# Optimization experiments

Hardware: AMD Instinct MI355X
Metric: run time of the kernel (lower is better)

The kernel has to match this reference:

```python
import jax, jax.numpy as jnp
import numpy as np

B, N, QD, OBJ_F, CONV_F = 16384, 6, 11, 10, 100
G_IN = 2 * CONV_F + QD  # 211


def _init_linear(key, fan_in, fan_out):
    kw, kb = jax.random.split(key)
    bound = 1.0 / np.sqrt(fan_in)
    W = jax.random.uniform(kw, (fan_in, fan_out), jnp.float32, -bound, bound)
    b = jax.random.uniform(kb, (fan_out,), jnp.float32, -bound, bound)
    return W, b


def setup_inputs() -> dict:
    key = jax.random.key(0)
    ks = jax.random.split(key, 13)
    tabs = jax.random.normal(ks[0], (B, N, OBJ_F), jnp.float32)
    qst = jax.random.normal(ks[1], (B, QD), jnp.float32)
    Wi1, bi1 = _init_linear(ks[2], 10, 256)
    Wi2, bi2 = _init_linear(ks[3], 256, 128)
    Wi3, bi3 = _init_linear(ks[4], 128, 100)
    Wg1, bg1 = _init_linear(ks[5], G_IN, 256)
    Wg2, bg2 = _init_linear(ks[6], 256, 256)
    Wg3, bg3 = _init_linear(ks[7], 256, 256)
    Wg4, bg4 = _init_linear(ks[8], 256, 256)
    Wf, bf = _init_linear(ks[9], 256, 256)
    Wo1, bo1 = _init_linear(ks[10], 256, 256)
    Wo2, bo2 = _init_linear(ks[11], 256, 10)
    return dict(tabs=tabs, qst=qst, Wi1=Wi1, bi1=bi1, Wi2=Wi2, bi2=bi2,
                Wi3=Wi3, bi3=bi3, Wg1=Wg1, bg1=bg1, Wg2=Wg2, bg2=bg2,
                Wg3=Wg3, bg3=bg3, Wg4=Wg4, bg4=bg4, Wf=Wf, bf=bf,
                Wo1=Wo1, bo1=bo1, Wo2=Wo2, bo2=bo2)


def reference(tabs, qst, Wi1, bi1, Wi2, bi2, Wi3, bi3,
              Wg1, bg1, Wg2, bg2, Wg3, bg3, Wg4, bg4,
              Wf, bf, Wo1, bo1, Wo2, bo2):
    relu = jax.nn.relu
    mb = tabs.shape[0]
    # object encoder: [B, N, 10] -> [B, N, 100]
    x = relu(tabs @ Wi1 + bi1)
    x = relu(x @ Wi2 + bi2)
    x = x @ Wi3 + bi3
    # x_j side carries the question: [B, N, 111]
    xq = jnp.concatenate([x, jnp.broadcast_to(qst[:, None, :], (mb, N, QD))], axis=-1)
    # pairwise features: pair (i, j) = [x[j], x[i], qst]  (matches torch repeat/cat)
    x_i = jnp.broadcast_to(x[:, None, :, :], (mb, N, N, CONV_F))
    x_j = jnp.broadcast_to(xq[:, :, None, :], (mb, N, N, CONV_F + QD))
    pair = jnp.concatenate([x_i, x_j], axis=-1).reshape(mb * N * N, G_IN)
    # g MLP over all pairs
    h = relu(pair @ Wg1 + bg1)
    h = relu(h @ Wg2 + bg2)
    h = relu(h @ Wg3 + bg3)
    h = relu(h @ Wg4 + bg4)
    # sum-pool over the 36 pairs
    g = h.reshape(mb, N * N, 256).sum(axis=1)
    # f MLP + output head (dropout treated as identity / eval mode)
    f = relu(g @ Wf + bf)
    o = relu(f @ Wo1 + bo1)
    logits = o @ Wo2 + bo2
    return jax.nn.log_softmax(logits, axis=1)
```

## Files before the change

### kernel.cpp

```cpp
#include <hip/hip_runtime.h>
#include <hip/hip_bf16.h>
#include <stdint.h>

typedef __attribute__((ext_vector_type(8))) __bf16 bf16x8;
typedef __attribute__((ext_vector_type(8))) short short8v;
typedef __attribute__((ext_vector_type(4))) short short4v;
typedef __attribute__((ext_vector_type(4))) float f32x4;
typedef __attribute__((ext_vector_type(2))) uint32_t u32x2;
typedef __attribute__((ext_vector_type(4))) uint32_t u32x4;

__device__ __forceinline__ float bf2f(short u) {
  return __builtin_bit_cast(float, (uint32_t)((uint32_t)(uint16_t)u << 16));
}
__device__ __forceinline__ short f2bf(float f) {
  uint32_t x = __builtin_bit_cast(uint32_t, f);
  x += 0x7FFFu + ((x >> 16) & 1u);
  return (short)(x >> 16);
}
__device__ __forceinline__ uint32_t cvtpk(float lo, float hi) {
  uint32_t r;
  asm("v_cvt_pk_bf16_f32 %0, %1, %2" : "=v"(r) : "v"(lo), "v"(hi));
  return r;
}
__device__ __forceinline__ f32x4 mfma16(short8v a, short8v b, f32x4 c) {
  return __builtin_amdgcn_mfma_f32_16x16x32_bf16(
      __builtin_bit_cast(bf16x8, a), __builtin_bit_cast(bf16x8, b), c, 0, 0, 0);
}
__device__ __forceinline__ int swz256(int row, int col) {
  return row * 256 + (col ^ ((row & 15) << 3));
}
__device__ __forceinline__ int swz128(int row, int col) {
  return row * 128 + (col ^ ((row & 15) << 3));
}

struct PPDesc { const float* src; short* dst; int Ks, Ns, KT, NT, tile_base; };
struct PPArgs { PPDesc d[11]; int n_desc; int total_tiles; };

__global__ void prepack_all(PPArgs args) {
  int idx = blockIdx.x * 256 + threadIdx.x;
  int tile = idx >> 6;
  if (tile >= args.total_tiles) return;
  int lane = idx & 63;
  int e = 0;
  while (e + 1 < args.n_desc && args.d[e + 1].tile_base <= tile) ++e;
  const PPDesc D = args.d[e];
  int t = tile - D.tile_base;
  int kt = t % D.KT, nt = t / D.KT;
  int n = nt * 16 + (lane & 15);
  int kbase = kt * 32 + ((lane >> 4) * 8);
  short8v o;
#pragma unroll
  for (int j = 0; j < 8; ++j) {
    int k = kbase + j;
    o[j] = f2bf((k < D.Ks && n < D.Ns) ? D.src[k * D.Ns + n] : 0.f);
  }
  *(short8v*)&D.dst[((size_t)t * 64 + lane) * 8] = o;
}

__global__ void qb_kernel(const float* __restrict__ qst, const float* __restrict__ Wg1,
                          const float* __restrict__ bg1, float* __restrict__ qb) {
  int c = threadIdx.x;
  int b0 = blockIdx.x * 32;
  float wcol[11];
#pragma unroll
  for (int k = 0; k < 11; ++k) wcol[k] = Wg1[(200 + k) * 256 + c];
  float bias = bg1[c];
#pragma unroll 1
  for (int bb = 0; bb < 32; ++bb) {
    int b = b0 + bb;
    float acc = bias;
#pragma unroll
    for (int k = 0; k < 11; ++k) acc += qst[b * 11 + k] * wcol[k];
    qb[b * 256 + c] = acc;
  }
}

__launch_bounds__(256, 3)
__global__ void enc_kernel(const float* __restrict__ tabs,
    const float* __restrict__ bi1, const float* __restrict__ bi2, const float* __restrict__ bi3,
    const short* __restrict__ Wi1p, const short* __restrict__ Wi2p, const short* __restrict__ Wi3p,
    const short* __restrict__ Wap, const short* __restrict__ Wbp,
    short* __restrict__ u_g, short* __restrict__ v_g) {
  __shared__ __align__(16) short sIn[64 * 32];
  __shared__ __align__(16) short sH1[64 * 256];
  __shared__ __align__(16) short sH2[64 * 128];
  short* sX = sH1;
  const int tid = threadIdx.x;
  const int lane = tid & 63, w = tid >> 6, quad = lane >> 4, ll = lane & 15;
  const int xl = ll << 3;
  const int obj0 = blockIdx.x * 64;

  for (int idx = tid; idx < 64 * 32; idx += 256) {
    int r = idx >> 5, k = idx & 31;
    float v = (k < 10) ? tabs[(obj0 + r) * 10 + k] : 0.f;
    sIn[idx] = f2bf(v);
  }
  __syncthreads();

  {
    f32x4 acc[4][4];
#pragma unroll
    for (int mi = 0; mi < 4; ++mi) {
      f32x4 b4 = *(const f32x4*)&bi1[(w * 4 + mi) * 16 + quad * 4];
#pragma unroll
      for (int nt = 0; nt < 4; ++nt) acc[mi][nt] = b4;
    }
    short8v wv[4];
#pragma unroll
    for (int mi = 0; mi < 4; ++mi)
      wv[mi] = *(const short8v*)&Wi1p[((w * 4 + mi) * 64 + lane) * 8];
#pragma unroll
    for (int nt = 0; nt < 4; ++nt) {
      short8v a = *(const short8v*)&sIn[(nt * 16 + ll) * 32 + quad * 8];
#pragma unroll
      for (int mi = 0; mi < 4; ++mi) acc[mi][nt] = mfma16(wv[mi], a, acc[mi][nt]);
    }
#pragma unroll
    for (int mi = 0; mi < 4; ++mi) {
      int c0 = (w * 4 + mi) * 16 + quad * 4;
#pragma unroll
      for (int nt = 0; nt < 4; ++nt) {
        int row = nt * 16 + ll;
        f32x4 a = acc[mi][nt];
        u32x2 o = {cvtpk(fmaxf(a[0], 0.f), fmaxf(a[1], 0.f)),
                   cvtpk(fmaxf(a[2], 0.f), fmaxf(a[3], 0.f))};
        *(u32x2*)&sH1[row * 256 + (c0 ^ ((row & 15) << 3))] = o;
      }
    }
  }
  __syncthreads();

  {
    f32x4 acc[2][4];
#pragma unroll
    for (int mi = 0; mi < 2; ++mi) {
      f32x4 b4 = *(const f32x4*)&bi2[(w * 2 + mi) * 16 + quad * 4];
#pragma unroll
      for (int nt = 0; nt < 4; ++nt) acc[mi][nt] = b4;
    }
#pragma unroll 1
    for (int kt = 0; kt < 8; ++kt) {
      short8v wv[2];
#pragma unroll
      for (int mi = 0; mi < 2; ++mi)
        wv[mi] = *(const short8v*)&Wi2p[(((w * 2 + mi) * 8 + kt) * 64 + lane) * 8];
#pragma unroll
      for (int nt = 0; nt < 4; ++nt) {
        short8v a = *(const short8v*)&sH1[(nt * 16 + ll) * 256 + ((kt * 32 + quad * 8) ^ xl)];
#pragma unroll
        for (int mi = 0; mi < 2; ++mi) acc[mi][nt] = mfma16(wv[mi], a, acc[mi][nt]);
      }
    }
    __syncthreads();
#pragma unroll
    for (int mi = 0; mi < 2; ++mi) {
      int c0 = (w * 2 + mi) * 16 + quad * 4;
#pragma unroll
      for (int nt = 0; nt < 4; ++nt) {
        int row = nt * 16 + ll;
        f32x4 a = acc[mi][nt];
        u32x2 o = {cvtpk(fmaxf(a[0], 0.f), fmaxf(a[1], 0.f)),
                   cvtpk(fmaxf(a[2], 0.f), fmaxf(a[3], 0.f))};
        *(u32x2*)&sH2[row * 128 + (c0 ^ ((row & 15) << 3))] = o;
      }
    }
  }
  __syncthreads();

  {
    f32x4 acc[4][2] = {};
#pragma unroll 1
    for (int kt = 0; kt < 4; ++kt) {
      short8v b[2];
#pragma unroll
      for (int ni = 0; ni < 2; ++ni)
        b[ni] = *(const short8v*)&Wi3p[(((w * 2 + ni) * 4 + kt) * 64 + lane) * 8];
#pragma unroll
      for (int mt = 0; mt < 4; ++mt) {
        short8v a = *(const short8v*)&sH2[(mt * 16 + ll) * 128 + ((kt * 32 + quad * 8) ^ xl)];
#pragma unroll
        for (int ni = 0; ni < 2; ++ni) acc[mt][ni] = mfma16(a, b[ni], acc[mt][ni]);
      }
    }
#pragma unroll
    for (int ni = 0; ni < 2; ++ni) {
      int col = (w * 2 + ni) * 16 + ll;
      float bias = (col < 100) ? bi3[col] : 0.f;
#pragma unroll
      for (int mt = 0; mt < 4; ++mt)
#pragma unroll
        for (int r = 0; r < 4; ++r) {
          int row = mt * 16 + quad * 4 + r;
          float vv = (col < 100) ? (acc[mt][ni][r] + bias) : 0.f;
          sX[swz128(row, col)] = f2bf(vv);
        }
    }
  }
  __syncthreads();

#pragma unroll 1
  for (int pass = 0; pass < 2; ++pass) {
    const short* Wp = pass ? Wbp : Wap;
    short* outg = pass ? v_g : u_g;
    f32x4 acc[4][4] = {};
#pragma unroll 1
    for (int kt = 0; kt < 4; ++kt) {
      short8v wv[4];
#pragma unroll
      for (int mi = 0; mi < 4; ++mi)
        wv[mi] = *(const short8v*)&Wp[(((w * 4 + mi) * 4 + kt) * 64 + lane) * 8];
#pragma unroll
      for (int nt = 0; nt < 4; ++nt) {
        short8v xb = *(const short8v*)&sX[(nt * 16 + ll) * 128 + ((kt * 32 + quad * 8) ^ xl)];
#pragma unroll
        for (int mi = 0; mi < 4; ++mi) acc[mi][nt] = mfma16(wv[mi], xb, acc[mi][nt]);
      }
    }
#pragma unroll
    for (int mi = 0; mi < 4; ++mi) {
      int c0 = (w * 4 + mi) * 16 + quad * 4;
#pragma unroll
      for (int nt = 0; nt < 4; ++nt) {
        int obj = obj0 + nt * 16 + ll;
        f32x4 a = acc[mi][nt];
        u32x2 o = {cvtpk(a[0], a[1]), cvtpk(a[2], a[3])};
        *(u32x2*)&outg[(size_t)obj * 256 + c0] = o;
      }
    }
  }
}

__launch_bounds__(512, 4)
__global__ void pair_kernel(const short* __restrict__ u_g, const short* __restrict__ v_g,
    const float* __restrict__ qbp,
    const short* __restrict__ Wg2p, const short* __restrict__ Wg3p, const short* __restrict__ Wg4p,
    const float* __restrict__ bg2, const float* __restrict__ bg3, const float* __restrict__ bg4,
    float* __restrict__ g_g) {
  __shared__ __align__(16) short sH[80 * 256];
  const int tid = threadIdx.x;
  const int lane = tid & 63, w = tid >> 6, quad = lane >> 4, ll = lane & 15;
  const int xl = ll << 3;
  const int b0 = blockIdx.x * 2;

  if (tid < 256) *(short8v*)&sH[72 * 256 + tid * 8] = short8v{};

#pragma unroll 1
  for (int it = 0; it < 5; ++it) {
    int vi = it * 512 + tid;
    if (vi < 2304) {
      int row = vi >> 5, c8 = (vi & 31) * 8;
      int bb = row / 36, p = row - bb * 36;
      int i2 = p / 6, j2 = p - i2 * 6;
      short8v u8 = *(const short8v*)&u_g[(size_t)((b0 + bb) * 6 + j2) * 256 + c8];
      short8v v8 = *(const short8v*)&v_g[(size_t)((b0 + bb) * 6 + i2) * 256 + c8];
      f32x4 qa = *(const f32x4*)&qbp[(size_t)(b0 + bb) * 256 + c8];
      f32x4 qc = *(const f32x4*)&qbp[(size_t)(b0 + bb) * 256 + c8 + 4];
      float m[8];
#pragma unroll
      for (int e = 0; e < 4; ++e) m[e] = fmaxf(bf2f(u8[e]) + bf2f(v8[e]) + qa[e], 0.f);
#pragma unroll
      for (int e = 0; e < 4; ++e) m[4 + e] = fmaxf(bf2f(u8[4 + e]) + bf2f(v8[4 + e]) + qc[e], 0.f);
      u32x4 o = {cvtpk(m[0], m[1]), cvtpk(m[2], m[3]), cvtpk(m[4], m[5]), cvtpk(m[6], m[7])};
      *(u32x4*)&sH[row * 256 + (c8 ^ ((row & 15) << 3))] = o;
    }
  }
  __syncthreads();

  f32x4 acc[5][2];

#pragma unroll 1
  for (int L = 0; L < 2; ++L) {
    const short* __restrict__ Wp = L ? Wg3p : Wg2p;
    const float* __restrict__ bp = L ? bg3 : bg2;
#pragma unroll
    for (int ni = 0; ni < 2; ++ni) {
      f32x4 b4 = *(const f32x4*)&bp[(w * 2 + ni) * 16 + quad * 4];
#pragma unroll
      for (int mt = 0; mt < 5; ++mt) acc[mt][ni] = b4;
    }
#pragma unroll 1
    for (int kt = 0; kt < 8; ++kt) {
      short8v wv[2];
#pragma unroll
      for (int ni = 0; ni < 2; ++ni)
        wv[ni] = *(const short8v*)&Wp[(((w * 2 + ni) * 8 + kt) * 64 + lane) * 8];
#pragma unroll
      for (int mt = 0; mt < 5; ++mt) {
        short8v h = *(const short8v*)&sH[(mt * 16 + ll) * 256 + ((kt * 32 + quad * 8) ^ xl)];
#pragma unroll
        for (int ni = 0; ni < 2; ++ni) acc[mt][ni] = mfma16(wv[ni], h, acc[mt][ni]);
      }
    }
    __syncthreads();
#pragma unroll
    for (int ni = 0; ni < 2; ++ni) {
      int c0 = (w * 2 + ni) * 16 + quad * 4;
#pragma unroll
      for (int mt = 0; mt < 5; ++mt) {
        int row = mt * 16 + ll;
        f32x4 a = acc[mt][ni];
        u32x2 o = {cvtpk(fmaxf(a[0], 0.f), fmaxf(a[1], 0.f)),
                   cvtpk(fmaxf(a[2], 0.f), fmaxf(a[3], 0.f))};
        *(u32x2*)&sH[row * 256 + (c0 ^ ((row & 15) << 3))] = o;
      }
    }
    __syncthreads();
  }

  {
#pragma unroll
    for (int ni = 0; ni < 2; ++ni) {
      float b = bg4[(w * 2 + ni) * 16 + ll];
#pragma unroll
      for (int mt = 0; mt < 5; ++mt) acc[mt][ni] = f32x4{b, b, b, b};
    }
#pragma unroll 1
    for (int kt = 0; kt < 8; ++kt) {
      short8v bv[2];
#pragma unroll
      for (int ni = 0; ni < 2; ++ni)
        bv[ni] = *(const short8v*)&Wg4p[(((w * 2 + ni) * 8 + kt) * 64 + lane) * 8];
#pragma unroll
      for (int mt = 0; mt < 5; ++mt) {
        short8v a = *(const short8v*)&sH[(mt * 16 + ll) * 256 + ((kt * 32 + quad * 8) ^ xl)];
#pragma unroll
        for (int ni = 0; ni < 2; ++ni) acc[mt][ni] = mfma16(a, bv[ni], acc[mt][ni]);
      }
    }
#pragma unroll
    for (int ni = 0; ni < 2; ++ni) {
      int col = (w * 2 + ni) * 16 + ll;
      float s0 = 0.f, s1 = 0.f;
#pragma unroll
      for (int mt = 0; mt < 5; ++mt) {
        int rbase = mt * 16 + quad * 4;
        float t = 0.f;
#pragma unroll
        for (int r = 0; r < 4; ++r) t += fmaxf(acc[mt][ni][r], 0.f);
        if (rbase < 36) s0 += t;
        else if (rbase < 72) s1 += t;
      }
      s0 += __shfl_xor(s0, 16, 64); s0 += __shfl_xor(s0, 32, 64);
      s1 += __shfl_xor(s1, 16, 64); s1 += __shfl_xor(s1, 32, 64);
      if (quad == 0) {
        g_g[(size_t)(b0 + 0) * 256 + col] = s0;
        g_g[(size_t)(b0 + 1) * 256 + col] = s1;
      }
    }
  }
}

template<int MT>
__device__ __forceinline__ void gemmMx256(const short* sInp, short* sOut,
    const short* __restrict__ Wp, const float* __restrict__ bias,
    int w, int lane, int quad, int ll, int xl) {
  f32x4 acc[MT][4] = {};
#pragma unroll 1
  for (int kt = 0; kt < 8; ++kt) {
    short8v b[4];
#pragma unroll
    for (int ni = 0; ni < 4; ++ni)
      b[ni] = *(const short8v*)&Wp[(((w * 4 + ni) * 8 + kt) * 64 + lane) * 8];
#pragma unroll
    for (int mt = 0; mt < MT; ++mt) {
      short8v a = *(const short8v*)&sInp[(mt * 16 + ll) * 256 + ((kt * 32 + quad * 8) ^ xl)];
#pragma unroll
      for (int ni = 0; ni < 4; ++ni) acc[mt][ni] = mfma16(a, b[ni], acc[mt][ni]);
    }
  }
#pragma unroll
  for (int ni = 0; ni < 4; ++ni) {
    int col = (w * 4 + ni) * 16 + ll;
    float bv = bias[col];
#pragma unroll
    for (int mt = 0; mt < MT; ++mt)
#pragma unroll
      for (int r = 0; r < 4; ++r) {
        int row = mt * 16 + quad * 4 + r;
        sOut[swz256(row, col)] = f2bf(fmaxf(acc[mt][ni][r] + bv, 0.f));
      }
  }
}

__launch_bounds__(256, 4)
__global__ void head_kernel(const float* __restrict__ g_g,
    const short* __restrict__ Wfp, const float* __restrict__ bf_,
    const short* __restrict__ Wo1p, const float* __restrict__ bo1,
    const short* __restrict__ Wo2p, const float* __restrict__ bo2,
    float* __restrict__ outp) {
  __shared__ __align__(16) short sA[32 * 256];
  __shared__ __align__(16) short sB[32 * 256];
  __shared__ float sL[32 * 16];
  const int tid = threadIdx.x;
  const int lane = tid & 63, w = tid >> 6, quad = lane >> 4, ll = lane & 15;
  const int xl = ll << 3;
  const int b0 = blockIdx.x * 32;

#pragma unroll 1
  for (int it = 0; it < 8; ++it) {
    int vi = it * 256 + tid;
    int row = vi >> 6, c4 = (vi & 63) * 4;
    f32x4 gv = *(const f32x4*)&g_g[(size_t)(b0 + row) * 256 + c4];
    short4v o;
#pragma unroll
    for (int e = 0; e < 4; ++e) o[e] = f2bf(gv[e]);
    *(short4v*)&sA[row * 256 + (c4 ^ ((row & 15) << 3))] = o;
  }
  __syncthreads();
  gemmMx256<2>(sA, sB, Wfp, bf_, w, lane, quad, ll, xl);
  __syncthreads();
  gemmMx256<2>(sB, sA, Wo1p, bo1, w, lane, quad, ll, xl);
  __syncthreads();
  if (w < 2) {
    f32x4 acc = {};
#pragma unroll 1
    for (int kt = 0; kt < 8; ++kt) {
      short8v b = *(const short8v*)&Wo2p[(kt * 64 + lane) * 8];
      short8v a = *(const short8v*)&sA[(w * 16 + ll) * 256 + ((kt * 32 + quad * 8) ^ xl)];
      acc = mfma16(a, b, acc);
    }
#pragma unroll
    for (int r = 0; r < 4; ++r) {
      int row = w * 16 + quad * 4 + r;
      sL[row * 16 + ll] = acc[r] + ((ll < 10) ? bo2[ll] : 0.f);
    }
  }
  __syncthreads();
  if (tid < 32) {
    float m = -1e30f;
#pragma unroll
    for (int c = 0; c < 10; ++c) m = fmaxf(m, sL[tid * 16 + c]);
    float s = 0.f;
#pragma unroll
    for (int c = 0; c < 10; ++c) s += expf(sL[tid * 16 + c] - m);
    float ls = logf(s) + m;
#pragma unroll
    for (int c = 0; c < 10; ++c) outp[(size_t)(b0 + tid) * 10 + c] = sL[tid * 16 + c] - ls;
  }
}

extern "C" void kernel_launch(void* const* d_in, const int* in_sizes, int n_in,
                              void* d_out, int out_size, void* d_ws, size_t ws_size,
                              hipStream_t stream) {
  const float* tabs = (const float*)d_in[0];
  const float* qst  = (const float*)d_in[1];
  const float* Wi1 = (const float*)d_in[2];  const float* bi1 = (const float*)d_in[3];
  const float* Wi2 = (const float*)d_in[4];  const float* bi2 = (const float*)d_in[5];
  const float* Wi3 = (const float*)d_in[6];  const float* bi3 = (const float*)d_in[7];
  const float* Wg1 = (const float*)d_in[8];  const float* bg1 = (const float*)d_in[9];
  const float* Wg2 = (const float*)d_in[10]; const float* bg2 = (const float*)d_in[11];
  const float* Wg3 = (const float*)d_in[12]; const float* bg3 = (const float*)d_in[13];
  const float* Wg4 = (const float*)d_in[14]; const float* bg4 = (const float*)d_in[15];
  const float* Wf  = (const float*)d_in[16]; const float* bf_ = (const float*)d_in[17];
  const float* Wo1 = (const float*)d_in[18]; const float* bo1 = (const float*)d_in[19];
  const float* Wo2 = (const float*)d_in[20]; const float* bo2 = (const float*)d_in[21];
  float* outp = (float*)d_out;
  (void)in_sizes; (void)n_in; (void)out_size; (void)ws_size;

  char* ws = (char*)d_ws;
  size_t off = 0;
  auto alloc = [&](size_t bytes) { void* p = ws + off; off += (bytes + 255) & ~(size_t)255; return p; };
  const size_t BN = 16384ull * 6;
  short* u_g = (short*)alloc(BN * 256 * 2);
  short* v_g = (short*)alloc(BN * 256 * 2);
  float* qb  = (float*)alloc(16384ull * 256 * 4);
  float* g_g = (float*)alloc(16384ull * 256 * 4);
  short* Wi1p = (short*)alloc(16 * 1 * 64 * 8 * 2);
  short* Wi2p = (short*)alloc(8 * 8 * 64 * 8 * 2);
  short* Wi3p = (short*)alloc(8 * 4 * 64 * 8 * 2);
  short* Wap  = (short*)alloc(16 * 4 * 64 * 8 * 2);
  short* Wbp  = (short*)alloc(16 * 4 * 64 * 8 * 2);
  short* Wg2p = (short*)alloc(16 * 8 * 64 * 8 * 2);
  short* Wg3p = (short*)alloc(16 * 8 * 64 * 8 * 2);
  short* Wg4p = (short*)alloc(16 * 8 * 64 * 8 * 2);
  short* Wfp  = (short*)alloc(16 * 8 * 64 * 8 * 2);
  short* Wo1p = (short*)alloc(16 * 8 * 64 * 8 * 2);
  short* Wo2p = (short*)alloc(1 * 8 * 64 * 8 * 2);

  PPArgs pa;
  int tb = 0, nd = 0;
  auto add = [&](const float* src, short* dst, int Ks, int Ns, int KT, int NT) {
    pa.d[nd++] = PPDesc{src, dst, Ks, Ns, KT, NT, tb};
    tb += KT * NT;
  };
  add(Wi1, Wi1p, 10, 256, 1, 16);
  add(Wi2, Wi2p, 256, 128, 8, 8);
  add(Wi3, Wi3p, 128, 100, 4, 8);
  add(Wg1,             Wap, 100, 256, 4, 16);
  add(Wg1 + 100 * 256, Wbp, 100, 256, 4, 16);
  add(Wg2, Wg2p, 256, 256, 8, 16);
  add(Wg3, Wg3p, 256, 256, 8, 16);
  add(Wg4, Wg4p, 256, 256, 8, 16);
  add(Wf,  Wfp,  256, 256, 8, 16);
  add(Wo1, Wo1p, 256, 256, 8, 16);
  add(Wo2, Wo2p, 256, 10, 8, 1);
  pa.n_desc = nd;
  pa.total_tiles = tb;
  prepack_all<<<(tb * 64 + 255) / 256, 256, 0, stream>>>(pa);

  qb_kernel<<<512, 256, 0, stream>>>(qst, Wg1, bg1, qb);
  enc_kernel<<<1536, 256, 0, stream>>>(tabs, bi1, bi2, bi3, Wi1p, Wi2p, Wi3p, Wap, Wbp, u_g, v_g);
  pair_kernel<<<8192, 512, 0, stream>>>(u_g, v_g, qb, Wg2p, Wg3p, Wg4p, bg2, bg3, bg4, g_g);
  head_kernel<<<512, 256, 0, stream>>>(g_g, Wfp, bf_, Wo1p, bo1, Wo2p, bo2, outp);
}
```

Measured before the change: 409.0 us.

## Process four batch items per pair-kernel block with 2x4 warp tiling

The pair kernel now handles four batch elements (two 80-row groups) per 512-thread block instead of two. Warps are split into two row groups and four column groups, each computing a 5x4 MFMA tile. This doubles the reuse of each loaded weight fragment and halves the number of weight loads per row. The cost is twice the shared memory (80 KB), more accumulator registers, and half as many blocks, which may reduce occupancy under the 512x4 launch bound.

```diff
diff --git a/kernel.cpp b/kernel.cpp
--- a/kernel.cpp
+++ b/kernel.cpp
@@ -236,68 +236,73 @@
     const short* __restrict__ Wg2p, const short* __restrict__ Wg3p, const short* __restrict__ Wg4p,
     const float* __restrict__ bg2, const float* __restrict__ bg3, const float* __restrict__ bg4,
     float* __restrict__ g_g) {
-  __shared__ __align__(16) short sH[80 * 256];
+  __shared__ __align__(16) short sH[160 * 256];
   const int tid = threadIdx.x;
   const int lane = tid & 63, w = tid >> 6, quad = lane >> 4, ll = lane & 15;
   const int xl = ll << 3;
-  const int b0 = blockIdx.x * 2;
-
-  if (tid < 256) *(short8v*)&sH[72 * 256 + tid * 8] = short8v{};
-
-#pragma unroll 1
-  for (int it = 0; it < 5; ++it) {
+  const int wg = w & 3, mg = w >> 2;
+  const int MT0 = mg * 5;
+  const int b0 = blockIdx.x * 4;
+
+  {
+    int pr = tid >> 5;
+    int row = (pr < 8) ? 72 + pr : 144 + pr;
+    *(short8v*)&sH[row * 256 + (tid & 31) * 8] = short8v{};
+  }
+
+#pragma unroll 1
+  for (int it = 0; it < 9; ++it) {
     int vi = it * 512 + tid;
-    if (vi < 2304) {
-      int row = vi >> 5, c8 = (vi & 31) * 8;
-      int bb = row / 36, p = row - bb * 36;
-      int i2 = p / 6, j2 = p - i2 * 6;
-      short8v u8 = *(const short8v*)&u_g[(size_t)((b0 + bb) * 6 + j2) * 256 + c8];
-      short8v v8 = *(const short8v*)&v_g[(size_t)((b0 + bb) * 6 + i2) * 256 + c8];
-      f32x4 qa = *(const f32x4*)&qbp[(size_t)(b0 + bb) * 256 + c8];
-      f32x4 qc = *(const f32x4*)&qbp[(size_t)(b0 + bb) * 256 + c8 + 4];
-      float m[8];
-#pragma unroll
-      for (int e = 0; e < 4; ++e) m[e] = fmaxf(bf2f(u8[e]) + bf2f(v8[e]) + qa[e], 0.f);
-#pragma unroll
-      for (int e = 0; e < 4; ++e) m[4 + e] = fmaxf(bf2f(u8[4 + e]) + bf2f(v8[4 + e]) + qc[e], 0.f);
-      u32x4 o = {cvtpk(m[0], m[1]), cvtpk(m[2], m[3]), cvtpk(m[4], m[5]), cvtpk(m[6], m[7])};
-      *(u32x4*)&sH[row * 256 + (c8 ^ ((row & 15) << 3))] = o;
-    }
-  }
-  __syncthreads();
-
-  f32x4 acc[5][2];
+    int row = vi >> 5, c8 = (vi & 31) * 8;
+    int bb = row / 36, p = row - bb * 36;
+    int i2 = p / 6, j2 = p - i2 * 6;
+    int prow = row + (row >= 72 ? 8 : 0);
+    short8v u8 = *(const short8v*)&u_g[(size_t)((b0 + bb) * 6 + j2) * 256 + c8];
+    short8v v8 = *(const short8v*)&v_g[(size_t)((b0 + bb) * 6 + i2) * 256 + c8];
+    f32x4 qa = *(const f32x4*)&qbp[(size_t)(b0 + bb) * 256 + c8];
+    f32x4 qc = *(const f32x4*)&qbp[(size_t)(b0 + bb) * 256 + c8 + 4];
+    float m[8];
+#pragma unroll
+    for (int e = 0; e < 4; ++e) m[e] = fmaxf(bf2f(u8[e]) + bf2f(v8[e]) + qa[e], 0.f);
+#pragma unroll
+    for (int e = 0; e < 4; ++e) m[4 + e] = fmaxf(bf2f(u8[4 + e]) + bf2f(v8[4 + e]) + qc[e], 0.f);
+    u32x4 o = {cvtpk(m[0], m[1]), cvtpk(m[2], m[3]), cvtpk(m[4], m[5]), cvtpk(m[6], m[7])};
+    *(u32x4*)&sH[prow * 256 + (c8 ^ ((prow & 15) << 3))] = o;
+  }
+  __syncthreads();
+
+  f32x4 acc[5][4];
 
 #pragma unroll 1
   for (int L = 0; L < 2; ++L) {
     const short* __restrict__ Wp = L ? Wg3p : Wg2p;
     const float* __restrict__ bp = L ? bg3 : bg2;
 #pragma unroll
-    for (int ni = 0; ni < 2; ++ni) {
-      f32x4 b4 = *(const f32x4*)&bp[(w * 2 + ni) * 16 + quad * 4];
+    for (int ni = 0; ni < 4; ++ni) {
+      f32x4 b4 = *(const f32x4*)&bp[(wg * 4 + ni) * 16 + quad * 4];
 #pragma unroll
       for (int mt = 0; mt < 5; ++mt) acc[mt][ni] = b4;
     }
 #pragma unroll 1
     for (int kt = 0; kt < 8; ++kt) {
-      short8v wv[2];
-#pragma unroll
-      for (int ni = 0; ni < 2; ++ni)
-        wv[ni] = *(const short8v*)&Wp[(((w * 2 + ni) * 8 + kt) * 64 + lane) * 8];
+      short8v wv[4];
+#pragma unroll
+      for (int ni = 0; ni < 4; ++ni)
+        wv[ni] = *(const short8v*)&Wp[(((wg * 4 + ni) * 8 + kt) * 64 + lane) * 8];
 #pragma unroll
       for (int mt = 0; mt < 5; ++mt) {
-        short8v h = *(const short8v*)&sH[(mt * 16 + ll) * 256 + ((kt * 32 + quad * 8) ^ xl)];
-#pragma unroll
-        for (int ni = 0; ni < 2; ++ni) acc[mt][ni] = mfma16(wv[ni], h, acc[mt][ni]);
+        short8v h = *(const short8v*)&sH[((MT0 + mt) * 16 + ll) * 256 + ((kt * 32 + quad * 8) ^ xl)];
+#pragma unroll
+        for (int ni = 0; ni < 4; ++ni) acc[mt][ni] = mfma16(wv[ni], h, acc[mt][ni]);
       }
     }
     __syncthreads();
 #pragma unroll
-    for (int ni = 0; ni < 2; ++ni) {
-      int c0 = (w * 2 + ni) * 16 + quad * 4;
+    for (int ni = 0; ni < 4; ++ni) {
+      int c0 = (wg * 4 + ni) * 16 + quad * 4;
 #pragma unroll
       for (int mt = 0; mt < 5; ++mt) {
-        int row = mt * 16 + ll;
+        int row = (MT0 + mt) * 16 + ll;
         f32x4 a = acc[mt][ni];
         u32x2 o = {cvtpk(fmaxf(a[0], 0.f), fmaxf(a[1], 0.f)),
                    cvtpk(fmaxf(a[2], 0.f), fmaxf(a[3], 0.f))};
@@ -309,42 +314,42 @@
 
   {
 #pragma unroll
-    for (int ni = 0; ni < 2; ++ni) {
-      float b = bg4[(w * 2 + ni) * 16 + ll];
+    for (int ni = 0; ni < 4; ++ni) {
+      float b = bg4[(wg * 4 + ni) * 16 + ll];
 #pragma unroll
       for (int mt = 0; mt < 5; ++mt) acc[mt][ni] = f32x4{b, b, b, b};
     }
 #pragma unroll 1
     for (int kt = 0; kt < 8; ++kt) {
-      short8v bv[2];
-#pragma unroll
-      for (int ni = 0; ni < 2; ++ni)
-        bv[ni] = *(const short8v*)&Wg4p[(((w * 2 + ni) * 8 + kt) * 64 + lane) * 8];
+      short8v bv[4];
+#pragma unroll
+      for (int ni = 0; ni < 4; ++ni)
+        bv[ni] = *(const short8v*)&Wg4p[(((wg * 4 + ni) * 8 + kt) * 64 + lane) * 8];
 #pragma unroll
       for (int mt = 0; mt < 5; ++mt) {
-        short8v a = *(const short8v*)&sH[(mt * 16 + ll) * 256 + ((kt * 32 + quad * 8) ^ xl)];
-#pragma unroll
-        for (int ni = 0; ni < 2; ++ni) acc[mt][ni] = mfma16(a, bv[ni], acc[mt][ni]);
-      }
-    }
-#pragma unroll
-    for (int ni = 0; ni < 2; ++ni) {
-      int col = (w * 2 + ni) * 16 + ll;
+        short8v a = *(const short8v*)&sH[((MT0 + mt) * 16 + ll) * 256 + ((kt * 32 + quad * 8) ^ xl)];
+#pragma unroll
+        for (int ni = 0; ni < 4; ++ni) acc[mt][ni] = mfma16(a, bv[ni], acc[mt][ni]);
+      }
+    }
+#pragma unroll
+    for (int ni = 0; ni < 4; ++ni) {
+      int col = (wg * 4 + ni) * 16 + ll;
       float s0 = 0.f, s1 = 0.f;
 #pragma unroll
       for (int mt = 0; mt < 5; ++mt) {
-        int rbase = mt * 16 + quad * 4;
+        int rr = mt * 16 + quad * 4;
         float t = 0.f;
 #pragma unroll
         for (int r = 0; r < 4; ++r) t += fmaxf(acc[mt][ni][r], 0.f);
-        if (rbase < 36) s0 += t;
-        else if (rbase < 72) s1 += t;
+        if (rr < 36) s0 += t;
+        else if (rr < 72) s1 += t;
       }
       s0 += __shfl_xor(s0, 16, 64); s0 += __shfl_xor(s0, 32, 64);
       s1 += __shfl_xor(s1, 16, 64); s1 += __shfl_xor(s1, 32, 64);
       if (quad == 0) {
-        g_g[(size_t)(b0 + 0) * 256 + col] = s0;
-        g_g[(size_t)(b0 + 1) * 256 + col] = s1;
+        g_g[(size_t)(b0 + mg * 2 + 0) * 256 + col] = s0;
+        g_g[(size_t)(b0 + mg * 2 + 1) * 256 + col] = s1;
       }
     }
   }
@@ -500,6 +505,6 @@
 
   qb_kernel<<<512, 256, 0, stream>>>(qst, Wg1, bg1, qb);
   enc_kernel<<<1536, 256, 0, stream>>>(tabs, bi1, bi2, bi3, Wi1p, Wi2p, Wi3p, Wap, Wbp, u_g, v_g);
-  pair_kernel<<<8192, 512, 0, stream>>>(u_g, v_g, qb, Wg2p, Wg3p, Wg4p, bg2, bg3, bg4, g_g);
+  pair_kernel<<<4096, 512, 0, stream>>>(u_g, v_g, qb, Wg2p, Wg3p, Wg4p, bg2, bg3, bg4, g_g);
   head_kernel<<<512, 256, 0, stream>>>(g_g, Wfp, bf_, Wo1p, bo1, Wo2p, bo2, outp);
 }
```

Measured after the change: 396.0 us. -3.2%, faster.
